# Optimization experiments

Hardware: AMD Instinct MI355X
Metric: run time of the kernel (lower is better)

Reference implementation:

```python
import jax, jax.numpy as jnp
import numpy as np

B, S, D = 8, 2048, 512
EPS = 1e-6
ROPE_THETA = 10000.0


def setup_inputs() -> dict:
    key = jax.random.key(0)
    ks = jax.random.split(key, 8)
    scale = 0.02
    return {
        "x": jax.random.normal(ks[0], (B, S, D), dtype=jnp.float32),
        "conv_w": jax.random.normal(ks[1], (D, D, 3), dtype=jnp.float32) * scale,
        "conv_b": jnp.zeros((D,), dtype=jnp.float32),
        "pre_g": jnp.ones((D,), dtype=jnp.float32),
        "q_g": jnp.ones((D,), dtype=jnp.float32),
        "k_g": jnp.ones((D,), dtype=jnp.float32),
        "Wq": jax.random.normal(ks[2], (D, D), dtype=jnp.float32) * scale,
        "Wk": jax.random.normal(ks[3], (D, D), dtype=jnp.float32) * scale,
        "Wv": jax.random.normal(ks[4], (D, D), dtype=jnp.float32) * scale,
    }


def _rmsnorm(x, g, eps=EPS):
    ms = jnp.mean(jnp.square(x), axis=-1, keepdims=True)
    return x * jax.lax.rsqrt(ms + eps) * g


def _rope_tables(seq_len, head_dim, dtype=jnp.float32):
    inv = 1.0 / (ROPE_THETA ** (jnp.arange(0, head_dim, 2, dtype=dtype) / head_dim))
    freqs = jnp.arange(seq_len, dtype=dtype)[:, None] * inv[None, :]  # [S, D/2]
    return jnp.cos(freqs), jnp.sin(freqs)


def _apply_rope(x, cos, sin):
    # x: [B, S, D]; treat last dim as D/2 complex pairs (interleaved real/imag)
    b, s, d = x.shape
    xr = x.reshape(b, s, d // 2, 2)
    x0, x1 = xr[..., 0], xr[..., 1]
    c = cos[None, :, :]
    sn = sin[None, :, :]
    o0 = x0 * c - x1 * sn
    o1 = x0 * sn + x1 * c
    return jnp.stack([o0, o1], axis=-1).reshape(b, s, d)


def reference(x, conv_w, conv_b, pre_g, q_g, k_g, Wq, Wk, Wv):
    b, s, d = x.shape
    # Conv1d over sequence axis (kernel 3, padding 1)
    xc = jnp.transpose(x, (0, 2, 1))  # [B, D, S]
    xc = jax.lax.conv_general_dilated(
        xc, conv_w, window_strides=(1,), padding=[(1, 1)],
        dimension_numbers=("NCH", "OIH", "NCH"))
    xc = xc + conv_b[None, :, None]
    x_norm = _rmsnorm(jnp.transpose(xc, (0, 2, 1)), pre_g)  # [B, S, D]

    q = _rmsnorm(jnp.einsum("bsd,ed->bse", x_norm, Wq), q_g)
    k = _rmsnorm(jnp.einsum("bsd,ed->bse", x_norm, Wk), k_g)
    v = jnp.einsum("bsd,ed->bse", x_norm, Wv)

    cos, sin = _rope_tables(s, d, x.dtype)
    q = _apply_rope(q, cos, sin)
    k = _apply_rope(k, cos, sin)

    scores = jnp.einsum("bqd,bkd->bqk", q, k) / jnp.sqrt(jnp.asarray(d, x.dtype))
    w = jax.nn.softmax(scores, axis=-1)  # dropout is identity in eval mode
    attended = jnp.einsum("bqk,bkd->bqd", w, v)
    out = x + attended
    return out.mean(axis=1)  # [B, D]
```

## Files before the change

kernel.cpp:

```cpp
#include <hip/hip_runtime.h>
#include <math.h>

#define BB 8
#define SS 2048
#define SSG 2050
#define DDIM 512
#define KC 1536
#define EPSV 1e-6f
#define SCALE 0.044194173824159216f

typedef unsigned short ushort_t;
using short8 = __attribute__((ext_vector_type(8))) short;
using f32x4  = __attribute__((ext_vector_type(4))) float;

__device__ inline unsigned short f2bf(float f) {
    union { float f; unsigned int u; } v; v.f = f;
    unsigned int r = v.u + 0x7FFFu + ((v.u >> 16) & 1u);
    return (unsigned short)(r >> 16);
}
__device__ inline unsigned int packbf(float a, float b) {
    return (unsigned int)f2bf(a) | ((unsigned int)f2bf(b) << 16);
}
__device__ inline float bf2f(unsigned short s) {
    union { unsigned int u; float f; } v; v.u = ((unsigned int)s) << 16; return v.f;
}

__device__ inline void gload16(const ushort_t* g, ushort_t* l) {
    __builtin_amdgcn_global_load_lds(
        (__attribute__((address_space(1))) const void*)g,
        (__attribute__((address_space(3))) void*)l, 16, 0, 0);
}

__device__ inline short8 ldswz(const ushort_t* s, int row, int c) {
    return *reinterpret_cast<const short8*>(&s[(row << 6) + ((c ^ (row & 7)) << 3)]);
}

__global__ __launch_bounds__(256) void kx_cast(const float* __restrict__ x,
                                               ushort_t* __restrict__ xbf,
                                               float* __restrict__ xsum)
{
    const int t = threadIdx.x;
    const int b = blockIdx.y;
    const int r0 = blockIdx.x * 16;
    const int c0 = 2 * t;
    if (blockIdx.x == 0) {
        *reinterpret_cast<unsigned int*>(&xbf[((size_t)b * SSG) * DDIM + c0]) = 0u;
        *reinterpret_cast<unsigned int*>(&xbf[((size_t)b * SSG + SS + 1) * DDIM + c0]) = 0u;
    }
    float s0 = 0.f, s1 = 0.f;
    for (int r = 0; r < 16; r++) {
        size_t srow = (size_t)b * SS + r0 + r;
        size_t drow = (size_t)b * SSG + 1 + r0 + r;
        float2 v = *reinterpret_cast<const float2*>(&x[srow * DDIM + c0]);
        s0 += v.x; s1 += v.y;
        *reinterpret_cast<unsigned int*>(&xbf[drow * DDIM + c0]) = packbf(v.x, v.y);
    }
    atomicAdd(&xsum[b * DDIM + c0], s0);
    atomicAdd(&xsum[b * DDIM + c0 + 1], s1);
}

__global__ __launch_bounds__(256) void k0_prep(
    const float* __restrict__ conv_w, const float* __restrict__ Wq,
    const float* __restrict__ Wk, const float* __restrict__ Wv,
    ushort_t* __restrict__ wcat, ushort_t* __restrict__ wqkv)
{
    int idx = blockIdx.x * 256 + threadIdx.x;
    {
        int o = idx / KC, kk = idx - o * KC;
        int t = kk >> 9, i = kk & 511;
        wcat[idx] = f2bf(conv_w[(size_t)o * KC + i * 3 + t]);
    }
    {
        int n = idx >> 9, d = idx & 511;
        const float* src = (n < 512) ? &Wq[(size_t)n * DDIM + d]
                         : (n < 1024) ? &Wk[(size_t)(n - 512) * DDIM + d]
                         : &Wv[(size_t)(n - 1024) * DDIM + d];
        wqkv[idx] = f2bf(*src);
    }
}

__global__ __launch_bounds__(256) void k1b_conv(
    const ushort_t* __restrict__ xbf, const ushort_t* __restrict__ wcat,
    const float* __restrict__ conv_b, ushort_t* __restrict__ ybf, float* __restrict__ rs)
{
    __shared__ alignas(16) ushort_t As[128 * 64];
    __shared__ alignas(16) ushort_t Bs[128 * 64];
    const int t = threadIdx.x;
    const int lane = t & 63, w = t >> 6;
    const int lm = lane & 15, lq = lane >> 4;
    const int wm = w >> 1, wn = w & 1;
    const int lr = lane >> 3;
    const int lc = ((lane & 7) ^ lr) << 3;
    const int s0 = blockIdx.x * 128;
    const int n0 = blockIdx.y * 128;
    const int b  = blockIdx.z;
    const ushort_t* Ag = xbf + (size_t)b * SSG * DDIM;
    const ushort_t* Bg = wcat + (size_t)n0 * KC;

    const ushort_t* pa[4]; const ushort_t* pb[4];
    ushort_t* da[4]; ushort_t* db[4];
    #pragma unroll
    for (int i = 0; i < 4; i++) {
        const int tr = (w * 4 + i) * 8 + lr;
        pa[i] = &Ag[(size_t)(s0 + tr) * DDIM + lc];
        pb[i] = &Bg[(size_t)tr * KC + lc];
        da[i] = &As[(w * 4 + i) * 512];
        db[i] = &Bs[(w * 4 + i) * 512];
    }

    f32x4 acc[4][4];
    #pragma unroll
    for (int i = 0; i < 4; i++)
        #pragma unroll
        for (int j = 0; j < 4; j++) acc[i][j] = (f32x4){0.f, 0.f, 0.f, 0.f};

    for (int dc = 0; dc < 24; dc++) {
        __syncthreads();
        const int koff = dc * 64;
        #pragma unroll
        for (int i = 0; i < 4; i++) {
            gload16(pa[i] + koff, da[i]);
            gload16(pb[i] + koff, db[i]);
        }
        __syncthreads();
        #pragma unroll
        for (int half = 0; half < 2; half++) {
            const int cb = (half << 2) | lq;
            short8 af0 = ldswz(As, wm * 64 +  0 + lm, cb);
            short8 af1 = ldswz(As, wm * 64 + 16 + lm, cb);
            short8 af2 = ldswz(As, wm * 64 + 32 + lm, cb);
            short8 af3 = ldswz(As, wm * 64 + 48 + lm, cb);
            #pragma unroll
            for (int nt = 0; nt < 4; nt++) {
                short8 bfv = ldswz(Bs, wn * 64 + nt * 16 + lm, cb);
                acc[0][nt] = __builtin_amdgcn_mfma_f32_16x16x32_bf16(af0, bfv, acc[0][nt], 0, 0, 0);
                acc[1][nt] = __builtin_amdgcn_mfma_f32_16x16x32_bf16(af1, bfv, acc[1][nt], 0, 0, 0);
                acc[2][nt] = __builtin_amdgcn_mfma_f32_16x16x32_bf16(af2, bfv, acc[2][nt], 0, 0, 0);
                acc[3][nt] = __builtin_amdgcn_mfma_f32_16x16x32_bf16(af3, bfv, acc[3][nt], 0, 0, 0);
            }
        }
    }

    const int rbase = s0 + wm * 64;
    const int cbase = n0 + wn * 64;
    ushort_t* yb = ybf + (size_t)b * SS * DDIM;
    float* rsb = rs + (size_t)b * SS;
    float bias[4];
    #pragma unroll
    for (int nt = 0; nt < 4; nt++) bias[nt] = conv_b[cbase + nt * 16 + lm];
    #pragma unroll
    for (int mt = 0; mt < 4; mt++) {
        float pr[4] = {0.f, 0.f, 0.f, 0.f};
        #pragma unroll
        for (int nt = 0; nt < 4; nt++) {
            #pragma unroll
            for (int r = 0; r < 4; r++) {
                float val = acc[mt][nt][r] + bias[nt];
                yb[(size_t)(rbase + mt * 16 + lq * 4 + r) * DDIM + cbase + nt * 16 + lm] = f2bf(val);
                pr[r] = fmaf(val, val, pr[r]);
            }
        }
        #pragma unroll
        for (int r = 0; r < 4; r++) {
            float p = pr[r];
            p += __shfl_xor(p, 1, 64); p += __shfl_xor(p, 2, 64);
            p += __shfl_xor(p, 4, 64); p += __shfl_xor(p, 8, 64);
            if (lm == 0) atomicAdd(&rsb[rbase + mt * 16 + lq * 4 + r], p);
        }
    }
}

__global__ __launch_bounds__(256) void k1n_norm(
    const ushort_t* __restrict__ ybf, const float* __restrict__ rs,
    const float* __restrict__ pre_g, ushort_t* __restrict__ xnbf)
{
    const int t = threadIdx.x;
    const int b = blockIdx.y;
    const int r0 = blockIdx.x * 8;
    float2 pg = *reinterpret_cast<const float2*>(&pre_g[2 * t]);
    for (int r = 0; r < 8; r++) {
        size_t row = (size_t)b * SS + r0 + r;
        float inv = rsqrtf(rs[row] * (1.0f / DDIM) + EPSV);
        unsigned int yv = *reinterpret_cast<const unsigned int*>(&ybf[row * DDIM + 2 * t]);
        float v0 = bf2f((ushort_t)(yv & 0xFFFF)), v1 = bf2f((ushort_t)(yv >> 16));
        *reinterpret_cast<unsigned int*>(&xnbf[row * DDIM + 2 * t]) =
            packbf(v0 * inv * pg.x, v1 * inv * pg.y);
    }
}

__global__ __launch_bounds__(256) void k1c_qkv(
    const ushort_t* __restrict__ xnbf, const ushort_t* __restrict__ wqkv,
    ushort_t* __restrict__ qraw, ushort_t* __restrict__ kraw, ushort_t* __restrict__ vb,
    float* __restrict__ rq, float* __restrict__ rk)
{
    __shared__ alignas(16) ushort_t As[128 * 64];
    __shared__ alignas(16) ushort_t Bs[128 * 64];
    const int t = threadIdx.x;
    const int lane = t & 63, w = t >> 6;
    const int lm = lane & 15, lq = lane >> 4;
    const int wm = w >> 1, wn = w & 1;
    const int lr = lane >> 3;
    const int lc = ((lane & 7) ^ lr) << 3;
    const int s0 = blockIdx.x * 128;
    const int n0 = blockIdx.y * 128;
    const int b  = blockIdx.z;
    const ushort_t* Ag = xnbf + ((size_t)b * SS + s0) * DDIM;
    const ushort_t* Bg = wqkv + (size_t)n0 * DDIM;

    const ushort_t* pa[4]; const ushort_t* pb[4];
    ushort_t* da[4]; ushort_t* db[4];
    #pragma unroll
    for (int i = 0; i < 4; i++) {
        const int tr = (w * 4 + i) * 8 + lr;
        pa[i] = &Ag[(size_t)tr * DDIM + lc];
        pb[i] = &Bg[(size_t)tr * DDIM + lc];
        da[i] = &As[(w * 4 + i) * 512];
        db[i] = &Bs[(w * 4 + i) * 512];
    }

    f32x4 acc[4][4];
    #pragma unroll
    for (int i = 0; i < 4; i++)
        #pragma unroll
        for (int j = 0; j < 4; j++) acc[i][j] = (f32x4){0.f, 0.f, 0.f, 0.f};

    for (int dc = 0; dc < 8; dc++) {
        __syncthreads();
        const int koff = dc * 64;
        #pragma unroll
        for (int i = 0; i < 4; i++) {
            gload16(pa[i] + koff, da[i]);
            gload16(pb[i] + koff, db[i]);
        }
        __syncthreads();
        #pragma unroll
        for (int half = 0; half < 2; half++) {
            const int cb = (half << 2) | lq;
            short8 af0 = ldswz(As, wm * 64 +  0 + lm, cb);
            short8 af1 = ldswz(As, wm * 64 + 16 + lm, cb);
            short8 af2 = ldswz(As, wm * 64 + 32 + lm, cb);
            short8 af3 = ldswz(As, wm * 64 + 48 + lm, cb);
            #pragma unroll
            for (int nt = 0; nt < 4; nt++) {
                short8 bfv = ldswz(Bs, wn * 64 + nt * 16 + lm, cb);
                acc[0][nt] = __builtin_amdgcn_mfma_f32_16x16x32_bf16(af0, bfv, acc[0][nt], 0, 0, 0);
                acc[1][nt] = __builtin_amdgcn_mfma_f32_16x16x32_bf16(af1, bfv, acc[1][nt], 0, 0, 0);
                acc[2][nt] = __builtin_amdgcn_mfma_f32_16x16x32_bf16(af2, bfv, acc[2][nt], 0, 0, 0);
                acc[3][nt] = __builtin_amdgcn_mfma_f32_16x16x32_bf16(af3, bfv, acc[3][nt], 0, 0, 0);
            }
        }
    }

    const int which = blockIdx.y >> 2;
    const int rbase = s0 + wm * 64;
    const int cbase = ((blockIdx.y & 3) * 128) + wn * 64;
    if (which == 2) {
        ushort_t* vbb = vb + (size_t)b * SS * DDIM;
        #pragma unroll
        for (int mt = 0; mt < 4; mt++)
            #pragma unroll
            for (int nt = 0; nt < 4; nt++)
                #pragma unroll
                for (int r = 0; r < 4; r++)
                    vbb[(size_t)(rbase + mt * 16 + lq * 4 + r) * DDIM + cbase + nt * 16 + lm] =
                        f2bf(acc[mt][nt][r]);
    } else {
        ushort_t* db2 = (which ? kraw : qraw) + (size_t)b * SS * DDIM;
        float* rb = (which ? rk : rq) + (size_t)b * SS;
        #pragma unroll
        for (int mt = 0; mt < 4; mt++) {
            float pr[4] = {0.f, 0.f, 0.f, 0.f};
            #pragma unroll
            for (int nt = 0; nt < 4; nt++) {
                #pragma unroll
                for (int r = 0; r < 4; r++) {
                    float val = acc[mt][nt][r];
                    db2[(size_t)(rbase + mt * 16 + lq * 4 + r) * DDIM + cbase + nt * 16 + lm] = f2bf(val);
                    pr[r] = fmaf(val, val, pr[r]);
                }
            }
            #pragma unroll
            for (int r = 0; r < 4; r++) {
                float p = pr[r];
                p += __shfl_xor(p, 1, 64); p += __shfl_xor(p, 2, 64);
                p += __shfl_xor(p, 4, 64); p += __shfl_xor(p, 8, 64);
                if (lm == 0) atomicAdd(&rb[rbase + mt * 16 + lq * 4 + r], p);
            }
        }
    }
}

__global__ __launch_bounds__(256) void k1d_rope(
    ushort_t* q_io, ushort_t* k_io,
    const float* __restrict__ rq, const float* __restrict__ rk,
    const float* __restrict__ q_g, const float* __restrict__ k_g)
{
    const int t = threadIdx.x;
    const int b = blockIdx.y;
    const int r0 = blockIdx.x * 8;
    const int c0 = 2 * t;
    float qg0 = q_g[c0], qg1 = q_g[c0 + 1];
    float kg0 = k_g[c0], kg1 = k_g[c0 + 1];
    float invf = (float)pow(10000.0, -(double)c0 / (double)DDIM);
    for (int r = 0; r < 8; r++) {
        int srow = r0 + r;
        size_t rowi = (size_t)b * SS + srow;
        float iq = rsqrtf(rq[rowi] * (1.0f / DDIM) + EPSV);
        float ik = rsqrtf(rk[rowi] * (1.0f / DDIM) + EPSV);
        size_t off = rowi * DDIM + c0;
        unsigned int qv = *reinterpret_cast<const unsigned int*>(&q_io[off]);
        unsigned int kv = *reinterpret_cast<const unsigned int*>(&k_io[off]);
        float q0 = bf2f((ushort_t)(qv & 0xFFFF)) * iq * qg0;
        float q1 = bf2f((ushort_t)(qv >> 16)) * iq * qg1;
        float k0v = bf2f((ushort_t)(kv & 0xFFFF)) * ik * kg0;
        float k1v = bf2f((ushort_t)(kv >> 16)) * ik * kg1;
        float ang = (float)srow * invf, sn, cs;
        sincosf(ang, &sn, &cs);
        *reinterpret_cast<unsigned int*>(&q_io[off]) = packbf(q0 * cs - q1 * sn, q0 * sn + q1 * cs);
        *reinterpret_cast<unsigned int*>(&k_io[off]) = packbf(k0v * cs - k1v * sn, k0v * sn + k1v * cs);
    }
}

__global__ __launch_bounds__(256) void k2a_rowsum(
    const ushort_t* __restrict__ qb, const ushort_t* __restrict__ kb,
    ushort_t* __restrict__ P, float* __restrict__ l)
{
    __shared__ alignas(16) ushort_t As[128 * 64];
    __shared__ alignas(16) ushort_t Bs[128 * 64];
    const int t = threadIdx.x;
    const int lane = t & 63, w = t >> 6;
    const int lm = lane & 15, lq = lane >> 4;
    const int wm = w >> 1, wn = w & 1;
    const int lr = lane >> 3;
    const int lc = ((lane & 7) ^ lr) << 3;
    const int b  = blockIdx.x;
    const int qt = blockIdx.y;
    const int kt = blockIdx.z;
    const ushort_t* Ag = qb + ((size_t)b * SS + qt * 128) * DDIM;
    const ushort_t* Bg = kb + ((size_t)b * SS + kt * 128) * DDIM;

    const ushort_t* pa[4]; const ushort_t* pb[4];
    ushort_t* da[4]; ushort_t* db[4];
    #pragma unroll
    for (int i = 0; i < 4; i++) {
        const int tr = (w * 4 + i) * 8 + lr;
        pa[i] = &Ag[(size_t)tr * DDIM + lc];
        pb[i] = &Bg[(size_t)tr * DDIM + lc];
        da[i] = &As[(w * 4 + i) * 512];
        db[i] = &Bs[(w * 4 + i) * 512];
    }

    f32x4 acc[4][4];
    #pragma unroll
    for (int i = 0; i < 4; i++)
        #pragma unroll
        for (int j = 0; j < 4; j++) acc[i][j] = (f32x4){0.f, 0.f, 0.f, 0.f};

    for (int dc = 0; dc < 8; dc++) {
        __syncthreads();
        const int koff = dc * 64;
        #pragma unroll
        for (int i = 0; i < 4; i++) {
            gload16(pa[i] + koff, da[i]);
            gload16(pb[i] + koff, db[i]);
        }
        __syncthreads();
        #pragma unroll
        for (int half = 0; half < 2; half++) {
            const int cb = (half << 2) | lq;
            short8 af0 = ldswz(As, wm * 64 +  0 + lm, cb);
            short8 af1 = ldswz(As, wm * 64 + 16 + lm, cb);
            short8 af2 = ldswz(As, wm * 64 + 32 + lm, cb);
            short8 af3 = ldswz(As, wm * 64 + 48 + lm, cb);
            #pragma unroll
            for (int nt = 0; nt < 4; nt++) {
                short8 bfv = ldswz(Bs, wn * 64 + nt * 16 + lm, cb);
                acc[0][nt] = __builtin_amdgcn_mfma_f32_16x16x32_bf16(af0, bfv, acc[0][nt], 0, 0, 0);
                acc[1][nt] = __builtin_amdgcn_mfma_f32_16x16x32_bf16(af1, bfv, acc[1][nt], 0, 0, 0);
                acc[2][nt] = __builtin_amdgcn_mfma_f32_16x16x32_bf16(af2, bfv, acc[2][nt], 0, 0, 0);
                acc[3][nt] = __builtin_amdgcn_mfma_f32_16x16x32_bf16(af3, bfv, acc[3][nt], 0, 0, 0);
            }
        }
    }

    const int rbase = qt * 128 + wm * 64;
    const int cbase = kt * 128 + wn * 64;
    ushort_t* Pb = P + (size_t)b * SS * SS;
    float* lrow = l + (size_t)b * SS;
    #pragma unroll
    for (int mt = 0; mt < 4; mt++) {
        #pragma unroll
        for (int r = 0; r < 4; r++) {
            const int row = rbase + mt * 16 + lq * 4 + r;
            float rowp = 0.f;
            #pragma unroll
            for (int nt = 0; nt < 4; nt++) {
                float e = __expf(acc[mt][nt][r] * SCALE);
                Pb[(size_t)row * SS + cbase + nt * 16 + lm] = f2bf(e);
                rowp += e;
            }
            float p = rowp;
            p += __shfl_xor(p, 1, 64); p += __shfl_xor(p, 2, 64);
            p += __shfl_xor(p, 4, 64); p += __shfl_xor(p, 8, 64);
            if (lm == 0) atomicAdd(&lrow[row], p);
        }
    }
}

__global__ __launch_bounds__(256) void k2c_colred(
    const ushort_t* __restrict__ P, const float* __restrict__ l,
    float* __restrict__ cw)
{
    const int t = threadIdx.x;
    const int b = blockIdx.z;
    const int k0 = blockIdx.x * 1024 + t * 4;
    const int q0 = blockIdx.y * 128;
    const ushort_t* Pb = P + ((size_t)b * SS + q0) * SS;
    const float* lb = l + (size_t)b * SS + q0;
    float a0 = 0.f, a1 = 0.f, a2 = 0.f, a3 = 0.f;
    for (int q = 0; q < 128; q++) {
        float rl = 1.0f / lb[q];
        uint2 pp = *reinterpret_cast<const uint2*>(&Pb[(size_t)q * SS + k0]);
        a0 = fmaf(bf2f((ushort_t)(pp.x & 0xFFFF)), rl, a0);
        a1 = fmaf(bf2f((ushort_t)(pp.x >> 16)), rl, a1);
        a2 = fmaf(bf2f((ushort_t)(pp.y & 0xFFFF)), rl, a2);
        a3 = fmaf(bf2f((ushort_t)(pp.y >> 16)), rl, a3);
    }
    atomicAdd(&cw[(size_t)b * SS + k0], a0);
    atomicAdd(&cw[(size_t)b * SS + k0 + 1], a1);
    atomicAdd(&cw[(size_t)b * SS + k0 + 2], a2);
    atomicAdd(&cw[(size_t)b * SS + k0 + 3], a3);
}

__global__ __launch_bounds__(256) void k4_out(
    const float* __restrict__ xsum, const ushort_t* __restrict__ v,
    const float* __restrict__ cwv, float* __restrict__ out)
{
    const int b = blockIdx.x, c = blockIdx.y;
    const int t = threadIdx.x;
    const int srow0 = c * (SS / 16);
    const ushort_t* vb = v + ((size_t)b * SS + srow0) * DDIM;
    const float* cwb   = cwv + (size_t)b * SS + srow0;
    float a0 = (c == 0) ? xsum[b * DDIM + t]       : 0.f;
    float a1 = (c == 0) ? xsum[b * DDIM + t + 256] : 0.f;
    for (int r = 0; r < SS / 16; r++) {
        float w = cwb[r];
        a0 += w * bf2f(vb[(size_t)r * DDIM + t]);
        a1 += w * bf2f(vb[(size_t)r * DDIM + t + 256]);
    }
    atomicAdd(&out[b * DDIM + t],       a0 * (1.0f / SS));
    atomicAdd(&out[b * DDIM + t + 256], a1 * (1.0f / SS));
}

extern "C" void kernel_launch(void* const* d_in, const int* in_sizes, int n_in,
                              void* d_out, int out_size, void* d_ws, size_t ws_size,
                              hipStream_t stream)
{
    const float* x      = (const float*)d_in[0];
    const float* conv_w = (const float*)d_in[1];
    const float* conv_b = (const float*)d_in[2];
    const float* pre_g  = (const float*)d_in[3];
    const float* q_g    = (const float*)d_in[4];
    const float* k_g    = (const float*)d_in[5];
    const float* Wq     = (const float*)d_in[6];
    const float* Wk     = (const float*)d_in[7];
    const float* Wv     = (const float*)d_in[8];
    float* out          = (float*)d_out;

    const size_t NTOK  = (size_t)BB * SS * DDIM;
    const size_t NTOKG = (size_t)BB * SSG * DDIM;
    char* p = (char*)d_ws;
    ushort_t* xbf = (ushort_t*)p; p += NTOKG * 2;
    ushort_t* ybf = (ushort_t*)p; p += NTOK * 2;
    ushort_t* xn  = (ushort_t*)p; p += NTOK * 2;
                         p += NTOK * 2;
    ushort_t* qio = (ushort_t*)p; p += NTOK * 2;
    ushort_t* kio = (ushort_t*)p; p += NTOK * 2;
    ushort_t* vb  = (ushort_t*)p; p += NTOK * 2;
    ushort_t* wcat = (ushort_t*)p; p += (size_t)DDIM * KC * 2;
    ushort_t* wqkv = (ushort_t*)p; p += (size_t)KC * DDIM * 2;
    float* rs   = (float*)p; p += (size_t)BB * SS * 4;
    float* rq   = (float*)p; p += (size_t)BB * SS * 4;
    float* rk   = (float*)p; p += (size_t)BB * SS * 4;
    float* lbuf = (float*)p; p += (size_t)BB * SS * 4;
    float* cwb  = (float*)p; p += (size_t)BB * SS * 4;
    float* xsum = (float*)p; p += (size_t)BB * DDIM * 4;

    ushort_t* Pbuf = xbf;

    (void)hipMemsetAsync(d_out, 0, (size_t)out_size * sizeof(float), stream);
    (void)hipMemsetAsync(rs, 0, ((size_t)BB * SS * 5 + (size_t)BB * DDIM) * sizeof(float), stream);

    kx_cast<<<dim3(SS / 16, BB), 256, 0, stream>>>(x, xbf, xsum);
    k0_prep<<<dim3(DDIM * KC / 256), 256, 0, stream>>>(conv_w, Wq, Wk, Wv, wcat, wqkv);
    k1b_conv<<<dim3(SS / 128, 4, BB), 256, 0, stream>>>(xbf, wcat, conv_b, ybf, rs);
    k1n_norm<<<dim3(SS / 8, BB), 256, 0, stream>>>(ybf, rs, pre_g, xn);
    k1c_qkv<<<dim3(SS / 128, 12, BB), 256, 0, stream>>>(xn, wqkv, qio, kio, vb, rq, rk);
    k1d_rope<<<dim3(SS / 8, BB), 256, 0, stream>>>(qio, kio, rq, rk, q_g, k_g);
    k2a_rowsum<<<dim3(BB, SS / 128, SS / 128), 256, 0, stream>>>(qio, kio, Pbuf, lbuf);
    k2c_colred<<<dim3(SS / 1024, SS / 128, BB), 256, 0, stream>>>(Pbuf, lbuf, cwb);
    k4_out<<<dim3(BB, 16), 256, 0, stream>>>(xsum, vb, cwb, out);
}
```

Baseline: 273.4 us.

## Pipeline GEMM kernels with 4-stage LDS ring and 128x256 tiles

Rewrites the three MFMA GEMM kernels (conv, QKV projection, QK^T scores) to use 512-thread blocks with 128x256 output tiles and a 4-slot LDS ring. Loads run three K-steps ahead with explicit vmcnt waits and raw s_barrier, and MFMA issue priority is raised. The aim is to overlap global-to-LDS loads with MFMA work and halve the block count. In exchange it uses more LDS and registers per block and relies on hand-tuned waitcnt values that must match the number of in-flight loads.

```diff
diff --git a/kernel.cpp b/kernel.cpp
--- a/kernel.cpp
+++ b/kernel.cpp
@@ -31,9 +31,37 @@
         (__attribute__((address_space(3))) void*)l, 16, 0, 0);
 }
 
-__device__ inline short8 ldswz(const ushort_t* s, int row, int c) {
-    return *reinterpret_cast<const short8*>(&s[(row << 6) + ((c ^ (row & 7)) << 3)]);
-}
+__device__ inline int gsw(int r) { return (r ^ (r >> 2)) & 3; }
+
+#define PIPE_HEAD(N) do { \
+    asm volatile("s_waitcnt vmcnt(" #N ")" ::: "memory"); \
+    __builtin_amdgcn_sched_barrier(0); \
+    __builtin_amdgcn_s_barrier(); \
+    asm volatile("" ::: "memory"); \
+    __builtin_amdgcn_sched_barrier(0); } while (0)
+
+#define PIPE_TAIL() do { \
+    asm volatile("s_waitcnt lgkmcnt(0)" ::: "memory"); \
+    __builtin_amdgcn_sched_barrier(0); \
+    __builtin_amdgcn_s_barrier(); \
+    asm volatile("" ::: "memory"); \
+    __builtin_amdgcn_sched_barrier(0); } while (0)
+
+#define PIPE_HEAD_SEL(ti, NT) do { \
+    if ((ti) < (NT) - 3)       PIPE_HEAD(9); \
+    else if ((ti) == (NT) - 3) PIPE_HEAD(6); \
+    else if ((ti) == (NT) - 2) PIPE_HEAD(3); \
+    else                       PIPE_HEAD(0); } while (0)
+
+#define MFMA16() do { \
+    __builtin_amdgcn_s_setprio(1); \
+    _Pragma("unroll") \
+    for (int nt = 0; nt < 4; nt++) { \
+        _Pragma("unroll") \
+        for (int mt = 0; mt < 4; mt++) \
+            acc[mt][nt] = __builtin_amdgcn_mfma_f32_16x16x32_bf16(av[mt], bv[nt], acc[mt][nt], 0, 0, 0); \
+    } \
+    __builtin_amdgcn_s_setprio(0); } while (0)
 
 __global__ __launch_bounds__(256) void kx_cast(const float* __restrict__ x,
                                                ushort_t* __restrict__ xbf,
@@ -79,33 +107,39 @@
     }
 }
 
-__global__ __launch_bounds__(256) void k1b_conv(
+__global__ __launch_bounds__(512, 2) void k1b_conv(
     const ushort_t* __restrict__ xbf, const ushort_t* __restrict__ wcat,
     const float* __restrict__ conv_b, ushort_t* __restrict__ ybf, float* __restrict__ rs)
 {
-    __shared__ alignas(16) ushort_t As[128 * 64];
-    __shared__ alignas(16) ushort_t Bs[128 * 64];
+    __shared__ alignas(16) ushort_t As[4][128 * 32];
+    __shared__ alignas(16) ushort_t Bs[4][256 * 32];
     const int t = threadIdx.x;
     const int lane = t & 63, w = t >> 6;
     const int lm = lane & 15, lq = lane >> 4;
-    const int wm = w >> 1, wn = w & 1;
-    const int lr = lane >> 3;
-    const int lc = ((lane & 7) ^ lr) << 3;
+    const int wm = w >> 2, wn = w & 3;
     const int s0 = blockIdx.x * 128;
-    const int n0 = blockIdx.y * 128;
+    const int n0 = blockIdx.y * 256;
     const int b  = blockIdx.z;
     const ushort_t* Ag = xbf + (size_t)b * SSG * DDIM;
     const ushort_t* Bg = wcat + (size_t)n0 * KC;
 
-    const ushort_t* pa[4]; const ushort_t* pb[4];
-    ushort_t* da[4]; ushort_t* db[4];
-    #pragma unroll
-    for (int i = 0; i < 4; i++) {
-        const int tr = (w * 4 + i) * 8 + lr;
-        pa[i] = &Ag[(size_t)(s0 + tr) * DDIM + lc];
-        pb[i] = &Bg[(size_t)tr * KC + lc];
-        da[i] = &As[(w * 4 + i) * 512];
-        db[i] = &Bs[(w * 4 + i) * 512];
+    const int rA  = w * 16 + (lane >> 2), pA = lane & 3;
+    const int rB0 = w * 32 + (lane >> 2), rB1 = rB0 + 16;
+    const ushort_t* pa0 = Ag + (size_t)(s0 + rA) * DDIM + (pA ^ gsw(rA)) * 8;
+    const ushort_t* pb0 = Bg + (size_t)rB0 * KC + (pA ^ gsw(rB0)) * 8;
+    const ushort_t* pb1 = Bg + (size_t)rB1 * KC + (pA ^ gsw(rB1)) * 8;
+    const int la0 = w * 512, lb0 = w * 1024, lb1 = w * 1024 + 512;
+
+    int oA[4], oB[4];
+    #pragma unroll
+    for (int mt = 0; mt < 4; mt++) {
+        int ra = wm * 64 + mt * 16 + lm;
+        oA[mt] = ra * 32 + (lq ^ gsw(ra)) * 8;
+    }
+    #pragma unroll
+    for (int nt = 0; nt < 4; nt++) {
+        int rb = wn * 64 + nt * 16 + lm;
+        oB[nt] = rb * 32 + (lq ^ gsw(rb)) * 8;
     }
 
     f32x4 acc[4][4];
@@ -114,32 +148,30 @@
         #pragma unroll
         for (int j = 0; j < 4; j++) acc[i][j] = (f32x4){0.f, 0.f, 0.f, 0.f};
 
-    for (int dc = 0; dc < 24; dc++) {
-        __syncthreads();
-        const int koff = dc * 64;
-        #pragma unroll
-        for (int i = 0; i < 4; i++) {
-            gload16(pa[i] + koff, da[i]);
-            gload16(pb[i] + koff, db[i]);
-        }
-        __syncthreads();
-        #pragma unroll
-        for (int half = 0; half < 2; half++) {
-            const int cb = (half << 2) | lq;
-            short8 af0 = ldswz(As, wm * 64 +  0 + lm, cb);
-            short8 af1 = ldswz(As, wm * 64 + 16 + lm, cb);
-            short8 af2 = ldswz(As, wm * 64 + 32 + lm, cb);
-            short8 af3 = ldswz(As, wm * 64 + 48 + lm, cb);
-            #pragma unroll
-            for (int nt = 0; nt < 4; nt++) {
-                short8 bfv = ldswz(Bs, wn * 64 + nt * 16 + lm, cb);
-                acc[0][nt] = __builtin_amdgcn_mfma_f32_16x16x32_bf16(af0, bfv, acc[0][nt], 0, 0, 0);
-                acc[1][nt] = __builtin_amdgcn_mfma_f32_16x16x32_bf16(af1, bfv, acc[1][nt], 0, 0, 0);
-                acc[2][nt] = __builtin_amdgcn_mfma_f32_16x16x32_bf16(af2, bfv, acc[2][nt], 0, 0, 0);
-                acc[3][nt] = __builtin_amdgcn_mfma_f32_16x16x32_bf16(af3, bfv, acc[3][nt], 0, 0, 0);
-            }
-        }
-    }
+    #define STG1B(tn, slab) do { \
+        int koA = (((tn) >> 4) << 9) + (((tn) & 15) << 5); \
+        int koB = (tn) << 5; \
+        gload16(pa0 + koA, &As[slab][la0]); \
+        gload16(pb0 + koB, &Bs[slab][lb0]); \
+        gload16(pb1 + koB, &Bs[slab][lb1]); } while (0)
+
+    STG1B(0, 0); STG1B(1, 1); STG1B(2, 2);
+    const int NT = 48;
+    for (int ti = 0; ti < NT; ++ti) {
+        const int rc = ti & 3;
+        if (ti + 3 < NT) STG1B(ti + 3, (ti + 3) & 3);
+        PIPE_HEAD_SEL(ti, NT);
+        const ushort_t* Acur = &As[rc][0];
+        const ushort_t* Bcur = &Bs[rc][0];
+        short8 av[4], bv[4];
+        #pragma unroll
+        for (int mt = 0; mt < 4; mt++) av[mt] = *reinterpret_cast<const short8*>(&Acur[oA[mt]]);
+        #pragma unroll
+        for (int nt = 0; nt < 4; nt++) bv[nt] = *reinterpret_cast<const short8*>(&Bcur[oB[nt]]);
+        MFMA16();
+        PIPE_TAIL();
+    }
+    #undef STG1B
 
     const int rbase = s0 + wm * 64;
     const int cbase = n0 + wn * 64;
@@ -188,34 +220,40 @@
     }
 }
 
-__global__ __launch_bounds__(256) void k1c_qkv(
+__global__ __launch_bounds__(512, 2) void k1c_qkv(
     const ushort_t* __restrict__ xnbf, const ushort_t* __restrict__ wqkv,
     ushort_t* __restrict__ qraw, ushort_t* __restrict__ kraw, ushort_t* __restrict__ vb,
     float* __restrict__ rq, float* __restrict__ rk)
 {
-    __shared__ alignas(16) ushort_t As[128 * 64];
-    __shared__ alignas(16) ushort_t Bs[128 * 64];
+    __shared__ alignas(16) ushort_t As[4][128 * 32];
+    __shared__ alignas(16) ushort_t Bs[4][256 * 32];
     const int t = threadIdx.x;
     const int lane = t & 63, w = t >> 6;
     const int lm = lane & 15, lq = lane >> 4;
-    const int wm = w >> 1, wn = w & 1;
-    const int lr = lane >> 3;
-    const int lc = ((lane & 7) ^ lr) << 3;
+    const int wm = w >> 2, wn = w & 3;
     const int s0 = blockIdx.x * 128;
-    const int n0 = blockIdx.y * 128;
+    const int n0 = blockIdx.y * 256;
     const int b  = blockIdx.z;
     const ushort_t* Ag = xnbf + ((size_t)b * SS + s0) * DDIM;
     const ushort_t* Bg = wqkv + (size_t)n0 * DDIM;
 
-    const ushort_t* pa[4]; const ushort_t* pb[4];
-    ushort_t* da[4]; ushort_t* db[4];
-    #pragma unroll
-    for (int i = 0; i < 4; i++) {
-        const int tr = (w * 4 + i) * 8 + lr;
-        pa[i] = &Ag[(size_t)tr * DDIM + lc];
-        pb[i] = &Bg[(size_t)tr * DDIM + lc];
-        da[i] = &As[(w * 4 + i) * 512];
-        db[i] = &Bs[(w * 4 + i) * 512];
+    const int rA  = w * 16 + (lane >> 2), pA = lane & 3;
+    const int rB0 = w * 32 + (lane >> 2), rB1 = rB0 + 16;
+    const ushort_t* pa0 = Ag + (size_t)rA * DDIM + (pA ^ gsw(rA)) * 8;
+    const ushort_t* pb0 = Bg + (size_t)rB0 * DDIM + (pA ^ gsw(rB0)) * 8;
+    const ushort_t* pb1 = Bg + (size_t)rB1 * DDIM + (pA ^ gsw(rB1)) * 8;
+    const int la0 = w * 512, lb0 = w * 1024, lb1 = w * 1024 + 512;
+
+    int oA[4], oB[4];
+    #pragma unroll
+    for (int mt = 0; mt < 4; mt++) {
+        int ra = wm * 64 + mt * 16 + lm;
+        oA[mt] = ra * 32 + (lq ^ gsw(ra)) * 8;
+    }
+    #pragma unroll
+    for (int nt = 0; nt < 4; nt++) {
+        int rb = wn * 64 + nt * 16 + lm;
+        oB[nt] = rb * 32 + (lq ^ gsw(rb)) * 8;
     }
 
     f32x4 acc[4][4];
@@ -224,36 +262,33 @@
         #pragma unroll
         for (int j = 0; j < 4; j++) acc[i][j] = (f32x4){0.f, 0.f, 0.f, 0.f};
 
-    for (int dc = 0; dc < 8; dc++) {
-        __syncthreads();
-        const int koff = dc * 64;
-        #pragma unroll
-        for (int i = 0; i < 4; i++) {
-            gload16(pa[i] + koff, da[i]);
-            gload16(pb[i] + koff, db[i]);
-        }
-        __syncthreads();
-        #pragma unroll
-        for (int half = 0; half < 2; half++) {
-            const int cb = (half << 2) | lq;
-            short8 af0 = ldswz(As, wm * 64 +  0 + lm, cb);
-            short8 af1 = ldswz(As, wm * 64 + 16 + lm, cb);
-            short8 af2 = ldswz(As, wm * 64 + 32 + lm, cb);
-            short8 af3 = ldswz(As, wm * 64 + 48 + lm, cb);
-            #pragma unroll
-            for (int nt = 0; nt < 4; nt++) {
-                short8 bfv = ldswz(Bs, wn * 64 + nt * 16 + lm, cb);
-                acc[0][nt] = __builtin_amdgcn_mfma_f32_16x16x32_bf16(af0, bfv, acc[0][nt], 0, 0, 0);
-                acc[1][nt] = __builtin_amdgcn_mfma_f32_16x16x32_bf16(af1, bfv, acc[1][nt], 0, 0, 0);
-                acc[2][nt] = __builtin_amdgcn_mfma_f32_16x16x32_bf16(af2, bfv, acc[2][nt], 0, 0, 0);
-                acc[3][nt] = __builtin_amdgcn_mfma_f32_16x16x32_bf16(af3, bfv, acc[3][nt], 0, 0, 0);
-            }
-        }
-    }
-
-    const int which = blockIdx.y >> 2;
+    #define STG1C(tn, slab) do { \
+        int ko = (tn) << 5; \
+        gload16(pa0 + ko, &As[slab][la0]); \
+        gload16(pb0 + ko, &Bs[slab][lb0]); \
+        gload16(pb1 + ko, &Bs[slab][lb1]); } while (0)
+
+    STG1C(0, 0); STG1C(1, 1); STG1C(2, 2);
+    const int NT = 16;
+    for (int ti = 0; ti < NT; ++ti) {
+        const int rc = ti & 3;
+        if (ti + 3 < NT) STG1C(ti + 3, (ti + 3) & 3);
+        PIPE_HEAD_SEL(ti, NT);
+        const ushort_t* Acur = &As[rc][0];
+        const ushort_t* Bcur = &Bs[rc][0];
+        short8 av[4], bv[4];
+        #pragma unroll
+        for (int mt = 0; mt < 4; mt++) av[mt] = *reinterpret_cast<const short8*>(&Acur[oA[mt]]);
+        #pragma unroll
+        for (int nt = 0; nt < 4; nt++) bv[nt] = *reinterpret_cast<const short8*>(&Bcur[oB[nt]]);
+        MFMA16();
+        PIPE_TAIL();
+    }
+    #undef STG1C
+
+    const int which = blockIdx.y >> 1;
     const int rbase = s0 + wm * 64;
-    const int cbase = ((blockIdx.y & 3) * 128) + wn * 64;
+    const int cbase = (blockIdx.y & 1) * 256 + wn * 64;
     if (which == 2) {
         ushort_t* vbb = vb + (size_t)b * SS * DDIM;
         #pragma unroll
@@ -321,33 +356,39 @@
     }
 }
 
-__global__ __launch_bounds__(256) void k2a_rowsum(
+__global__ __launch_bounds__(512, 2) void k2a_rowsum(
     const ushort_t* __restrict__ qb, const ushort_t* __restrict__ kb,
     ushort_t* __restrict__ P, float* __restrict__ l)
 {
-    __shared__ alignas(16) ushort_t As[128 * 64];
-    __shared__ alignas(16) ushort_t Bs[128 * 64];
+    __shared__ alignas(16) ushort_t As[4][128 * 32];
+    __shared__ alignas(16) ushort_t Bs[4][256 * 32];
     const int t = threadIdx.x;
     const int lane = t & 63, w = t >> 6;
     const int lm = lane & 15, lq = lane >> 4;
-    const int wm = w >> 1, wn = w & 1;
-    const int lr = lane >> 3;
-    const int lc = ((lane & 7) ^ lr) << 3;
-    const int b  = blockIdx.x;
-    const int qt = blockIdx.y;
-    const int kt = blockIdx.z;
+    const int wm = w >> 2, wn = w & 3;
+    const int b   = blockIdx.x;
+    const int qt  = blockIdx.y;
+    const int ktb = blockIdx.z;
     const ushort_t* Ag = qb + ((size_t)b * SS + qt * 128) * DDIM;
-    const ushort_t* Bg = kb + ((size_t)b * SS + kt * 128) * DDIM;
-
-    const ushort_t* pa[4]; const ushort_t* pb[4];
-    ushort_t* da[4]; ushort_t* db[4];
-    #pragma unroll
-    for (int i = 0; i < 4; i++) {
-        const int tr = (w * 4 + i) * 8 + lr;
-        pa[i] = &Ag[(size_t)tr * DDIM + lc];
-        pb[i] = &Bg[(size_t)tr * DDIM + lc];
-        da[i] = &As[(w * 4 + i) * 512];
-        db[i] = &Bs[(w * 4 + i) * 512];
+    const ushort_t* Bg = kb + ((size_t)b * SS + ktb * 256) * DDIM;
+
+    const int rA  = w * 16 + (lane >> 2), pA = lane & 3;
+    const int rB0 = w * 32 + (lane >> 2), rB1 = rB0 + 16;
+    const ushort_t* pa0 = Ag + (size_t)rA * DDIM + (pA ^ gsw(rA)) * 8;
+    const ushort_t* pb0 = Bg + (size_t)rB0 * DDIM + (pA ^ gsw(rB0)) * 8;
+    const ushort_t* pb1 = Bg + (size_t)rB1 * DDIM + (pA ^ gsw(rB1)) * 8;
+    const int la0 = w * 512, lb0 = w * 1024, lb1 = w * 1024 + 512;
+
+    int oA[4], oB[4];
+    #pragma unroll
+    for (int mt = 0; mt < 4; mt++) {
+        int ra = wm * 64 + mt * 16 + lm;
+        oA[mt] = ra * 32 + (lq ^ gsw(ra)) * 8;
+    }
+    #pragma unroll
+    for (int nt = 0; nt < 4; nt++) {
+        int rb = wn * 64 + nt * 16 + lm;
+        oB[nt] = rb * 32 + (lq ^ gsw(rb)) * 8;
     }
 
     f32x4 acc[4][4];
@@ -356,35 +397,32 @@
         #pragma unroll
         for (int j = 0; j < 4; j++) acc[i][j] = (f32x4){0.f, 0.f, 0.f, 0.f};
 
-    for (int dc = 0; dc < 8; dc++) {
-        __syncthreads();
-        const int koff = dc * 64;
-        #pragma unroll
-        for (int i = 0; i < 4; i++) {
-            gload16(pa[i] + koff, da[i]);
-            gload16(pb[i] + koff, db[i]);
-        }
-        __syncthreads();
-        #pragma unroll
-        for (int half = 0; half < 2; half++) {
-            const int cb = (half << 2) | lq;
-            short8 af0 = ldswz(As, wm * 64 +  0 + lm, cb);
-            short8 af1 = ldswz(As, wm * 64 + 16 + lm, cb);
-            short8 af2 = ldswz(As, wm * 64 + 32 + lm, cb);
-            short8 af3 = ldswz(As, wm * 64 + 48 + lm, cb);
-            #pragma unroll
-            for (int nt = 0; nt < 4; nt++) {
-                short8 bfv = ldswz(Bs, wn * 64 + nt * 16 + lm, cb);
-                acc[0][nt] = __builtin_amdgcn_mfma_f32_16x16x32_bf16(af0, bfv, acc[0][nt], 0, 0, 0);
-                acc[1][nt] = __builtin_amdgcn_mfma_f32_16x16x32_bf16(af1, bfv, acc[1][nt], 0, 0, 0);
-                acc[2][nt] = __builtin_amdgcn_mfma_f32_16x16x32_bf16(af2, bfv, acc[2][nt], 0, 0, 0);
-                acc[3][nt] = __builtin_amdgcn_mfma_f32_16x16x32_bf16(af3, bfv, acc[3][nt], 0, 0, 0);
-            }
-        }
-    }
+    #define STG2A(tn, slab) do { \
+        int ko = (tn) << 5; \
+        gload16(pa0 + ko, &As[slab][la0]); \
+        gload16(pb0 + ko, &Bs[slab][lb0]); \
+        gload16(pb1 + ko, &Bs[slab][lb1]); } while (0)
+
+    STG2A(0, 0); STG2A(1, 1); STG2A(2, 2);
+    const int NT = 16;
+    for (int ti = 0; ti < NT; ++ti) {
+        const int rc = ti & 3;
+        if (ti + 3 < NT) STG2A(ti + 3, (ti + 3) & 3);
+        PIPE_HEAD_SEL(ti, NT);
+        const ushort_t* Acur = &As[rc][0];
+        const ushort_t* Bcur = &Bs[rc][0];
+        short8 av[4], bv[4];
+        #pragma unroll
+        for (int mt = 0; mt < 4; mt++) av[mt] = *reinterpret_cast<const short8*>(&Acur[oA[mt]]);
+        #pragma unroll
+        for (int nt = 0; nt < 4; nt++) bv[nt] = *reinterpret_cast<const short8*>(&Bcur[oB[nt]]);
+        MFMA16();
+        PIPE_TAIL();
+    }
+    #undef STG2A
 
     const int rbase = qt * 128 + wm * 64;
-    const int cbase = kt * 128 + wn * 64;
+    const int cbase = ktb * 256 + wn * 64;
     ushort_t* Pb = P + (size_t)b * SS * SS;
     float* lrow = l + (size_t)b * SS;
     #pragma unroll
@@ -493,11 +531,11 @@
 
     kx_cast<<<dim3(SS / 16, BB), 256, 0, stream>>>(x, xbf, xsum);
     k0_prep<<<dim3(DDIM * KC / 256), 256, 0, stream>>>(conv_w, Wq, Wk, Wv, wcat, wqkv);
-    k1b_conv<<<dim3(SS / 128, 4, BB), 256, 0, stream>>>(xbf, wcat, conv_b, ybf, rs);
+    k1b_conv<<<dim3(SS / 128, 2, BB), 512, 0, stream>>>(xbf, wcat, conv_b, ybf, rs);
     k1n_norm<<<dim3(SS / 8, BB), 256, 0, stream>>>(ybf, rs, pre_g, xn);
-    k1c_qkv<<<dim3(SS / 128, 12, BB), 256, 0, stream>>>(xn, wqkv, qio, kio, vb, rq, rk);
+    k1c_qkv<<<dim3(SS / 128, 6, BB), 512, 0, stream>>>(xn, wqkv, qio, kio, vb, rq, rk);
     k1d_rope<<<dim3(SS / 8, BB), 256, 0, stream>>>(qio, kio, rq, rk, q_g, k_g);
-    k2a_rowsum<<<dim3(BB, SS / 128, SS / 128), 256, 0, stream>>>(qio, kio, Pbuf, lbuf);
+    k2a_rowsum<<<dim3(BB, SS / 128, SS / 256), 512, 0, stream>>>(qio, kio, Pbuf, lbuf);
     k2c_colred<<<dim3(SS / 1024, SS / 128, BB), 256, 0, stream>>>(Pbuf, lbuf, cwb);
     k4_out<<<dim3(BB, 16), 256, 0, stream>>>(xsum, vb, cwb, out);
 }
```

Result: slower. 325.9 us (+19.2%).

## Double-buffer LDS tiles in conv, QKV and score GEMM kernels

Applied to the files above, without the earlier changes.

Gives the three MFMA GEMM kernels two LDS buffers each for A and B, so global-to-LDS loads for the next K tile are issued before computing the current tile, and only one barrier is needed per iteration. The aim is to hide global load latency behind MFMA work. LDS use per block doubles to 64KB, which can lower occupancy. Correctness depends on gload16 being an async direct-to-LDS load whose completion is covered by the barrier.

```diff
diff --git a/kernel.cpp b/kernel.cpp
--- a/kernel.cpp
+++ b/kernel.cpp
@@ -79,12 +79,30 @@
     }
 }
 
+#define COMPUTE_TILE(Acur, Bcur) do { \
+    _Pragma("unroll") \
+    for (int half = 0; half < 2; half++) { \
+        const int cb = (half << 2) | lq; \
+        short8 af0 = ldswz(Acur, wm * 64 +  0 + lm, cb); \
+        short8 af1 = ldswz(Acur, wm * 64 + 16 + lm, cb); \
+        short8 af2 = ldswz(Acur, wm * 64 + 32 + lm, cb); \
+        short8 af3 = ldswz(Acur, wm * 64 + 48 + lm, cb); \
+        _Pragma("unroll") \
+        for (int nt = 0; nt < 4; nt++) { \
+            short8 bfv = ldswz(Bcur, wn * 64 + nt * 16 + lm, cb); \
+            acc[0][nt] = __builtin_amdgcn_mfma_f32_16x16x32_bf16(af0, bfv, acc[0][nt], 0, 0, 0); \
+            acc[1][nt] = __builtin_amdgcn_mfma_f32_16x16x32_bf16(af1, bfv, acc[1][nt], 0, 0, 0); \
+            acc[2][nt] = __builtin_amdgcn_mfma_f32_16x16x32_bf16(af2, bfv, acc[2][nt], 0, 0, 0); \
+            acc[3][nt] = __builtin_amdgcn_mfma_f32_16x16x32_bf16(af3, bfv, acc[3][nt], 0, 0, 0); \
+        } \
+    } } while (0)
+
 __global__ __launch_bounds__(256) void k1b_conv(
     const ushort_t* __restrict__ xbf, const ushort_t* __restrict__ wcat,
     const float* __restrict__ conv_b, ushort_t* __restrict__ ybf, float* __restrict__ rs)
 {
-    __shared__ alignas(16) ushort_t As[128 * 64];
-    __shared__ alignas(16) ushort_t Bs[128 * 64];
+    __shared__ alignas(16) ushort_t As[2][128 * 64];
+    __shared__ alignas(16) ushort_t Bs[2][128 * 64];
     const int t = threadIdx.x;
     const int lane = t & 63, w = t >> 6;
     const int lm = lane & 15, lq = lane >> 4;
@@ -98,14 +116,13 @@
     const ushort_t* Bg = wcat + (size_t)n0 * KC;
 
     const ushort_t* pa[4]; const ushort_t* pb[4];
-    ushort_t* da[4]; ushort_t* db[4];
+    int la[4];
     #pragma unroll
     for (int i = 0; i < 4; i++) {
         const int tr = (w * 4 + i) * 8 + lr;
         pa[i] = &Ag[(size_t)(s0 + tr) * DDIM + lc];
         pb[i] = &Bg[(size_t)tr * KC + lc];
-        da[i] = &As[(w * 4 + i) * 512];
-        db[i] = &Bs[(w * 4 + i) * 512];
+        la[i] = (w * 4 + i) * 512;
     }
 
     f32x4 acc[4][4];
@@ -114,32 +131,24 @@
         #pragma unroll
         for (int j = 0; j < 4; j++) acc[i][j] = (f32x4){0.f, 0.f, 0.f, 0.f};
 
-    for (int dc = 0; dc < 24; dc++) {
+    #define STG1B(tn, bufi) do { \
+        const int koA = (tn) * 64; \
+        _Pragma("unroll") \
+        for (int i = 0; i < 4; i++) { \
+            gload16(pa[i] + koA, &As[bufi][la[i]]); \
+            gload16(pb[i] + koA, &Bs[bufi][la[i]]); \
+        } } while (0)
+
+    const int NT = 24;
+    STG1B(0, 0);
+    __syncthreads();
+    for (int dc = 0; dc < NT; dc++) {
+        const int cur = dc & 1;
+        if (dc + 1 < NT) STG1B(dc + 1, cur ^ 1);
+        COMPUTE_TILE(&As[cur][0], &Bs[cur][0]);
         __syncthreads();
-        const int koff = dc * 64;
-        #pragma unroll
-        for (int i = 0; i < 4; i++) {
-            gload16(pa[i] + koff, da[i]);
-            gload16(pb[i] + koff, db[i]);
-        }
-        __syncthreads();
-        #pragma unroll
-        for (int half = 0; half < 2; half++) {
-            const int cb = (half << 2) | lq;
-            short8 af0 = ldswz(As, wm * 64 +  0 + lm, cb);
-            short8 af1 = ldswz(As, wm * 64 + 16 + lm, cb);
-            short8 af2 = ldswz(As, wm * 64 + 32 + lm, cb);
-            short8 af3 = ldswz(As, wm * 64 + 48 + lm, cb);
-            #pragma unroll
-            for (int nt = 0; nt < 4; nt++) {
-                short8 bfv = ldswz(Bs, wn * 64 + nt * 16 + lm, cb);
-                acc[0][nt] = __builtin_amdgcn_mfma_f32_16x16x32_bf16(af0, bfv, acc[0][nt], 0, 0, 0);
-                acc[1][nt] = __builtin_amdgcn_mfma_f32_16x16x32_bf16(af1, bfv, acc[1][nt], 0, 0, 0);
-                acc[2][nt] = __builtin_amdgcn_mfma_f32_16x16x32_bf16(af2, bfv, acc[2][nt], 0, 0, 0);
-                acc[3][nt] = __builtin_amdgcn_mfma_f32_16x16x32_bf16(af3, bfv, acc[3][nt], 0, 0, 0);
-            }
-        }
-    }
+    }
+    #undef STG1B
 
     const int rbase = s0 + wm * 64;
     const int cbase = n0 + wn * 64;
@@ -193,8 +202,8 @@
     ushort_t* __restrict__ qraw, ushort_t* __restrict__ kraw, ushort_t* __restrict__ vb,
     float* __restrict__ rq, float* __restrict__ rk)
 {
-    __shared__ alignas(16) ushort_t As[128 * 64];
-    __shared__ alignas(16) ushort_t Bs[128 * 64];
+    __shared__ alignas(16) ushort_t As[2][128 * 64];
+    __shared__ alignas(16) ushort_t Bs[2][128 * 64];
     const int t = threadIdx.x;
     const int lane = t & 63, w = t >> 6;
     const int lm = lane & 15, lq = lane >> 4;
@@ -208,14 +217,13 @@
     const ushort_t* Bg = wqkv + (size_t)n0 * DDIM;
 
     const ushort_t* pa[4]; const ushort_t* pb[4];
-    ushort_t* da[4]; ushort_t* db[4];
+    int la[4];
     #pragma unroll
     for (int i = 0; i < 4; i++) {
         const int tr = (w * 4 + i) * 8 + lr;
         pa[i] = &Ag[(size_t)tr * DDIM + lc];
         pb[i] = &Bg[(size_t)tr * DDIM + lc];
-        da[i] = &As[(w * 4 + i) * 512];
-        db[i] = &Bs[(w * 4 + i) * 512];
+        la[i] = (w * 4 + i) * 512;
     }
 
     f32x4 acc[4][4];
@@ -224,32 +232,24 @@
         #pragma unroll
         for (int j = 0; j < 4; j++) acc[i][j] = (f32x4){0.f, 0.f, 0.f, 0.f};
 
-    for (int dc = 0; dc < 8; dc++) {
+    #define STG1C(tn, bufi) do { \
+        const int ko = (tn) * 64; \
+        _Pragma("unroll") \
+        for (int i = 0; i < 4; i++) { \
+            gload16(pa[i] + ko, &As[bufi][la[i]]); \
+            gload16(pb[i] + ko, &Bs[bufi][la[i]]); \
+        } } while (0)
+
+    const int NT = 8;
+    STG1C(0, 0);
+    __syncthreads();
+    for (int dc = 0; dc < NT; dc++) {
+        const int cur = dc & 1;
+        if (dc + 1 < NT) STG1C(dc + 1, cur ^ 1);
+        COMPUTE_TILE(&As[cur][0], &Bs[cur][0]);
         __syncthreads();
-        const int koff = dc * 64;
-        #pragma unroll
-        for (int i = 0; i < 4; i++) {
-            gload16(pa[i] + koff, da[i]);
-            gload16(pb[i] + koff, db[i]);
-        }
-        __syncthreads();
-        #pragma unroll
-        for (int half = 0; half < 2; half++) {
-            const int cb = (half << 2) | lq;
-            short8 af0 = ldswz(As, wm * 64 +  0 + lm, cb);
-            short8 af1 = ldswz(As, wm * 64 + 16 + lm, cb);
-            short8 af2 = ldswz(As, wm * 64 + 32 + lm, cb);
-            short8 af3 = ldswz(As, wm * 64 + 48 + lm, cb);
-            #pragma unroll
-            for (int nt = 0; nt < 4; nt++) {
-                short8 bfv = ldswz(Bs, wn * 64 + nt * 16 + lm, cb);
-                acc[0][nt] = __builtin_amdgcn_mfma_f32_16x16x32_bf16(af0, bfv, acc[0][nt], 0, 0, 0);
-                acc[1][nt] = __builtin_amdgcn_mfma_f32_16x16x32_bf16(af1, bfv, acc[1][nt], 0, 0, 0);
-                acc[2][nt] = __builtin_amdgcn_mfma_f32_16x16x32_bf16(af2, bfv, acc[2][nt], 0, 0, 0);
-                acc[3][nt] = __builtin_amdgcn_mfma_f32_16x16x32_bf16(af3, bfv, acc[3][nt], 0, 0, 0);
-            }
-        }
-    }
+    }
+    #undef STG1C
 
     const int which = blockIdx.y >> 2;
     const int rbase = s0 + wm * 64;
@@ -325,8 +325,8 @@
     const ushort_t* __restrict__ qb, const ushort_t* __restrict__ kb,
     ushort_t* __restrict__ P, float* __restrict__ l)
 {
-    __shared__ alignas(16) ushort_t As[128 * 64];
-    __shared__ alignas(16) ushort_t Bs[128 * 64];
+    __shared__ alignas(16) ushort_t As[2][128 * 64];
+    __shared__ alignas(16) ushort_t Bs[2][128 * 64];
     const int t = threadIdx.x;
     const int lane = t & 63, w = t >> 6;
     const int lm = lane & 15, lq = lane >> 4;
@@ -340,14 +340,13 @@
     const ushort_t* Bg = kb + ((size_t)b * SS + kt * 128) * DDIM;
 
     const ushort_t* pa[4]; const ushort_t* pb[4];
-    ushort_t* da[4]; ushort_t* db[4];
+    int la[4];
     #pragma unroll
     for (int i = 0; i < 4; i++) {
         const int tr = (w * 4 + i) * 8 + lr;
         pa[i] = &Ag[(size_t)tr * DDIM + lc];
         pb[i] = &Bg[(size_t)tr * DDIM + lc];
-        da[i] = &As[(w * 4 + i) * 512];
-        db[i] = &Bs[(w * 4 + i) * 512];
+        la[i] = (w * 4 + i) * 512;
     }
 
     f32x4 acc[4][4];
@@ -356,32 +355,24 @@
         #pragma unroll
         for (int j = 0; j < 4; j++) acc[i][j] = (f32x4){0.f, 0.f, 0.f, 0.f};
 
-    for (int dc = 0; dc < 8; dc++) {
+    #define STG2A(tn, bufi) do { \
+        const int ko = (tn) * 64; \
+        _Pragma("unroll") \
+        for (int i = 0; i < 4; i++) { \
+            gload16(pa[i] + ko, &As[bufi][la[i]]); \
+            gload16(pb[i] + ko, &Bs[bufi][la[i]]); \
+        } } while (0)
+
+    const int NT = 8;
+    STG2A(0, 0);
+    __syncthreads();
+    for (int dc = 0; dc < NT; dc++) {
+        const int cur = dc & 1;
+        if (dc + 1 < NT) STG2A(dc + 1, cur ^ 1);
+        COMPUTE_TILE(&As[cur][0], &Bs[cur][0]);
         __syncthreads();
-        const int koff = dc * 64;
-        #pragma unroll
-        for (int i = 0; i < 4; i++) {
-            gload16(pa[i] + koff, da[i]);
-            gload16(pb[i] + koff, db[i]);
-        }
-        __syncthreads();
-        #pragma unroll
-        for (int half = 0; half < 2; half++) {
-            const int cb = (half << 2) | lq;
-            short8 af0 = ldswz(As, wm * 64 +  0 + lm, cb);
-            short8 af1 = ldswz(As, wm * 64 + 16 + lm, cb);
-            short8 af2 = ldswz(As, wm * 64 + 32 + lm, cb);
-            short8 af3 = ldswz(As, wm * 64 + 48 + lm, cb);
-            #pragma unroll
-            for (int nt = 0; nt < 4; nt++) {
-                short8 bfv = ldswz(Bs, wn * 64 + nt * 16 + lm, cb);
-                acc[0][nt] = __builtin_amdgcn_mfma_f32_16x16x32_bf16(af0, bfv, acc[0][nt], 0, 0, 0);
-                acc[1][nt] = __builtin_amdgcn_mfma_f32_16x16x32_bf16(af1, bfv, acc[1][nt], 0, 0, 0);
-                acc[2][nt] = __builtin_amdgcn_mfma_f32_16x16x32_bf16(af2, bfv, acc[2][nt], 0, 0, 0);
-                acc[3][nt] = __builtin_amdgcn_mfma_f32_16x16x32_bf16(af3, bfv, acc[3][nt], 0, 0, 0);
-            }
-        }
-    }
+    }
+    #undef STG2A
 
     const int rbase = qt * 128 + wm * 64;
     const int cbase = kt * 128 + wn * 64;
```

Result: slower. 284.0 us (+3.9%).
